# Optimization experiments

Measured on AMD Instinct MI355X. Metric: run time of the kernel, lower is better.

Reference implementation:

```python
import jax, jax.numpy as jnp
import numpy as np

B, N, HID, EPOCH = 16, 512, 32, 201


def setup_inputs() -> dict:
    key = jax.random.key(0)
    k1, k2, k3, k4 = jax.random.split(key, 4)
    f = jax.random.normal(k1, (B, 1, N, N), dtype=jnp.float32)
    # per-sample 3x3 stencil: perturbed 5-point Laplacian, positive center for stable Jacobi
    base = jnp.array([[0., -1., 0.], [-1., 4., -1.], [0., -1., 0.]], dtype=jnp.float32)
    kernelA = base[None, None] + 0.1 * jax.random.normal(k2, (B, 1, 3, 3), dtype=jnp.float32)
    kernelA = kernelA.at[:, :, 1, 1].set(jnp.maximum(kernelA[:, :, 1, 1], 1.0))
    u = jnp.zeros((B, 1, N, N), jnp.float32)
    # stand-in DeepONet H: pointwise 2 -> HID -> 1 MLP on concat(LFA, residual)
    W1 = 0.1 * jax.random.normal(k3, (HID, 2), dtype=jnp.float32)
    b1 = jnp.zeros((HID,), jnp.float32)
    W2 = 0.1 * jax.random.normal(k4, (1, HID), dtype=jnp.float32)
    b2 = jnp.zeros((1,), jnp.float32)
    return {"f": f, "kernelA": kernelA, "u": u, "W1": W1, "b1": b1, "W2": W2, "b2": b2, "epoch": EPOCH}


def _A(x, kernel):
    # per-sample 3x3 stencil: batch dim mapped to channels, grouped conv (groups = B)
    bsz = x.shape[0]
    y = jax.lax.conv_general_dilated(
        jnp.transpose(x, (1, 0, 2, 3)), kernel, (1, 1), ((1, 1), (1, 1)),
        dimension_numbers=("NCHW", "OIHW", "NCHW"), feature_group_count=bsz)
    return jnp.transpose(y, (1, 0, 2, 3))


def _lfa(kernelA, n):
    # ComputeSmootherFactor: Jacobi symbol |prod_j (1 - tau * A_hat(theta))| on the frequency grid
    h = 1.0 / (n + 1)
    p = np.arange(-(n // 2), n // 2)
    P1, P2 = np.meshgrid(p, p)
    t1 = jnp.asarray(2j * np.pi * h * P1, jnp.complex64)
    t2 = jnp.asarray(2j * np.pi * h * P2, jnp.complex64)
    E = jnp.stack([
        jnp.exp(-t1 - t2), jnp.exp(-t2), jnp.exp(t1 - t2),
        jnp.exp(-t1), jnp.ones_like(t1), jnp.exp(t1),
        jnp.exp(-t1 + t2), jnp.exp(t2), jnp.exp(t1 + t2)])  # [9,N,N]
    bsz = kernelA.shape[0]
    S = jnp.einsum("bk,kxy->bxy", kernelA.reshape(bsz, 9).astype(jnp.complex64), E)
    tau = (0.5 / kernelA[:, 0, 1, 1]).astype(jnp.complex64)[:, None, None]
    y = (1.0 - tau * S) ** 5  # 5 identical Jacobi factors
    return jnp.abs(y)[:, None].astype(jnp.float32)  # [B,1,N,N]


def _H(lfa, r, W1, b1, W2, b2):
    # pointwise MLP correction operator (stand-in for DeepONet)
    z = jnp.concatenate([lfa, r], axis=1)  # [B,2,N,N]
    hdn = jax.nn.gelu(jnp.einsum("bcxy,oc->boxy", z, W1) + b1[None, :, None, None])
    return jnp.einsum("bcxy,oc->boxy", hdn, W2) + b2[None, :, None, None]


def reference(f, kernelA, u, W1, b1, W2, b2, epoch):
    K = (epoch - 1) // 100 + 1
    n = f.shape[-1]
    lfa = _lfa(kernelA, n)
    taus = 0.5 / kernelA[:, :, 1:2, 1:2]  # [B,1,1,1], w=0.5
    x = jnp.zeros_like(f)
    for _ in range(K):
        for _ in range(10):  # jacobi, M=10
            x = x + taus * (f - _A(x, kernelA))
        r = f - _A(x, kernelA)
        x = x + _H(lfa, r, W1, b1, W2, b2)
    r = f - _A(x, kernelA)
    return jnp.linalg.norm(r) / jnp.linalg.norm(f)
```

## Files before the change

kernel.cpp:

```cpp
#include <hip/hip_runtime.h>
#include <math.h>

#define BB 16
#define NN 512
#define HID 32

#define HALO 16
#define TW 96
#define TWP 97
#define OT 64

#define GELU_K1 (-2.302208201f)
#define GELU_K2 (-0.102944244f)

#define TPH 0.012247925f
#define CDR 0.99992499f
#define SDR 0.012247618f

template <bool FIRST, bool RES>
__global__ __launch_bounds__(256) void fused_cycle(
        const float* __restrict__ xin, float* __restrict__ xout,
        const float* __restrict__ f, const float* __restrict__ kernelA,
        float* __restrict__ lfa,
        const float* __restrict__ W1, const float* __restrict__ b1,
        const float* __restrict__ W2, const float* __restrict__ b2,
        float* __restrict__ accp) {
    __shared__ float sxraw[98 * TWP + 2];
    float* sx = sxraw + TWP + 1;
    const int tx = threadIdx.x;
    const int ty = threadIdx.y;
    const int t  = ty * 32 + tx;
    const int b  = blockIdx.z;
    const int gy0 = blockIdx.y * OT;
    const int gx0 = blockIdx.x * OT;
    const int goi = gy0 - HALO;
    const int goj = gx0 - HALO;
    const float* fg = f + (size_t)b * NN * NN;
    const float* ag = kernelA + b * 9;
    const float ar0 = ag[0], ar1 = ag[1], ar2 = ag[2], ar3 = ag[3], ar4 = ag[4];
    const float ar5 = ag[5], ar6 = ag[6], ar7 = ag[7], ar8 = ag[8];
    const float tau = 0.5f / ar4;
    const float s0 = tau * ar0, q1 = tau * ar1, q2 = tau * ar2, q3 = tau * ar3;
    const float q4 = tau * ar4, q5 = tau * ar5, q6 = tau * ar6, q7 = tau * ar7;
    const float q8 = tau * ar8;

    if (FIRST) {
        if (t == 0 && (blockIdx.x | blockIdx.y | blockIdx.z) == 0) {
            accp[0] = 0.f;
            accp[1] = 0.f;
        }
        const int orw = t >> 2;
        const int osg = t & 3;
        const int gi_ = gy0 + orw;
        const int gj_ = gx0 + osg * 16;
        const float A35 = ar3 + ar5, A17 = ar1 + ar7, A08 = ar0 + ar8, A26 = ar2 + ar6;
        const float B53 = ar5 - ar3, B71 = ar7 - ar1, B80 = ar8 - ar0, B26 = ar2 - ar6;
        float th2 = TPH * (float)(gi_ - NN / 2);
        float s2v, c2v;
        sincosf(th2, &s2v, &c2v);
        float* lrow = lfa + (size_t)b * NN * NN + (size_t)gi_ * NN + gj_;
        for (int g = 0; g < 4; ++g) {
            float th1 = TPH * (float)(gj_ + g * 4 - NN / 2);
            float s1, c1;
            sincosf(th1, &s1, &c1);
            float out[4];
#pragma unroll
            for (int k = 0; k < 4; ++k) {
                float cc = c1 * c2v, ss = s1 * s2v, sc = s1 * c2v, cs = c1 * s2v;
                float cpp = cc - ss, cpm = cc + ss, spp = sc + cs, spm = sc - cs;
                float re = fmaf(A35, c1, ar4); re = fmaf(A17, c2v, re);
                re = fmaf(A08, cpp, re);       re = fmaf(A26, cpm, re);
                float im = B53 * s1;           im = fmaf(B71, s2v, im);
                im = fmaf(B80, spp, im);       im = fmaf(B26, spm, im);
                float zre = fmaf(-tau, re, 1.0f);
                float zim = tau * im;
                float m2 = fmaf(zre, zre, zim * zim);
                out[k] = m2 * m2 * sqrtf(m2);
                float tt = s1 * SDR;
                float ns = fmaf(s1, CDR, c1 * SDR);
                c1 = fmaf(c1, CDR, -tt);
                s1 = ns;
            }
            float4 ov = {out[0], out[1], out[2], out[3]};
            *(float4*)(lrow + g * 4) = ov;
        }
    }

    if (t < 98) sxraw[t] = 0.f;
    if (t < 96) sxraw[97 + 97 * t] = 0.f;
    if (t < 98) sxraw[9409 + t] = 0.f;

    if (!FIRST) {
        const float* xg = xin + (size_t)b * NN * NN;
#pragma unroll
        for (int k = 0; k < (TW * TW) / 256; ++k) {
            int idx = t + k * 256;
            int row = idx / TW, col = idx - row * TW;
            int gi = goi + row, gj = goj + col;
            float v = 0.f;
            if (gi >= 0 && gi < NN && gj >= 0 && gj < NN) v = xg[gi * NN + gj];
            sx[row * TWP + col] = v;
        }
    }

    const int R0 = ty * 12, C0 = tx * 3;

    const float* pb  = sx + (R0 - 1) * TWP + (C0 - 1);
    float*       pwv = sx + R0 * TWP + C0;

    float vR[12], vC[3];
#pragma unroll
    for (int r = 0; r < 12; ++r) {
        int R = R0 + r, gi = goi + R;
        vR[r] = (R >= 1 && R < TW - 1 && gi >= 0 && gi < NN) ? 1.f : 0.f;
    }
#pragma unroll
    for (int c = 0; c < 3; ++c) {
        int C = C0 + c, gj = goj + C;
        vC[c] = (C >= 1 && C < TW - 1 && gj >= 0 && gj < NN) ? 1.f : 0.f;
    }

    float frt[12][3];
#pragma unroll
    for (int r = 0; r < 12; ++r) {
        int gi = goi + R0 + r;
#pragma unroll
        for (int c = 0; c < 3; ++c) {
            int gj = goj + C0 + c;
            frt[r][c] = (gi >= 0 && gi < NN && gj >= 0 && gj < NN)
                            ? tau * fg[gi * NN + gj] : 0.f;
        }
    }

    __syncthreads();

    float cur[12][3];
    if (FIRST) {
#pragma unroll
        for (int r = 0; r < 12; ++r) {
#pragma unroll
            for (int c = 0; c < 3; ++c)
                cur[r][c] = (vR[r] * vC[c]) * frt[r][c];
        }
        pwv[0] = cur[0][0]; pwv[1] = cur[0][1]; pwv[2] = cur[0][2];
        pwv[11 * TWP] = cur[11][0]; pwv[11 * TWP + 1] = cur[11][1];
        pwv[11 * TWP + 2] = cur[11][2];
#pragma unroll
        for (int r = 1; r < 11; ++r) {
            pwv[r * TWP] = cur[r][0];
            pwv[r * TWP + 2] = cur[r][2];
        }
        __syncthreads();
    } else {
#pragma unroll
        for (int r = 0; r < 12; ++r) {
            cur[r][0] = pwv[r * TWP];
            cur[r][1] = pwv[r * TWP + 1];
            cur[r][2] = pwv[r * TWP + 2];
        }
    }

    for (int s = FIRST ? 1 : 0; s < 10; ++s) {
        float top0 = pb[0], top1 = pb[1], top2 = pb[2], top3 = pb[3], top4 = pb[4];
        float bot0 = pb[13 * TWP],     bot1 = pb[13 * TWP + 1],
              bot2 = pb[13 * TWP + 2], bot3 = pb[13 * TWP + 3],
              bot4 = pb[13 * TWP + 4];
        float pm0 = top1, pm1v = top2, pm2 = top3;
        float Lm1 = top0, Rm1 = top4;
        float Lc = pb[TWP], Rc = pb[TWP + 4];
#pragma unroll
        for (int r = 0; r < 12; ++r) {
            float n0, n1, n2, Lp, Rp;
            if (r < 11) {
                n0 = cur[r + 1][0]; n1 = cur[r + 1][1]; n2 = cur[r + 1][2];
                Lp = pb[(r + 2) * TWP];
                Rp = pb[(r + 2) * TWP + 4];
            } else {
                n0 = bot1; n1 = bot2; n2 = bot3; Lp = bot0; Rp = bot4;
            }
            float o0 = cur[r][0], o1 = cur[r][1], o2 = cur[r][2];
            {
                float ax = s0 * Lm1;
                ax = fmaf(q1, pm0, ax); ax = fmaf(q2, pm1v, ax);
                ax = fmaf(q3, Lc, ax);  ax = fmaf(q4, o0, ax);
                ax = fmaf(q5, o1, ax);  ax = fmaf(q6, Lp, ax);
                ax = fmaf(q7, n0, ax);  ax = fmaf(q8, n1, ax);
                cur[r][0] = fmaf(vR[r] * vC[0], frt[r][0] - ax, o0);
            }
            {
                float ax = s0 * pm0;
                ax = fmaf(q1, pm1v, ax); ax = fmaf(q2, pm2, ax);
                ax = fmaf(q3, o0, ax);   ax = fmaf(q4, o1, ax);
                ax = fmaf(q5, o2, ax);   ax = fmaf(q6, n0, ax);
                ax = fmaf(q7, n1, ax);   ax = fmaf(q8, n2, ax);
                cur[r][1] = fmaf(vR[r] * vC[1], frt[r][1] - ax, o1);
            }
            {
                float ax = s0 * pm1v;
                ax = fmaf(q1, pm2, ax); ax = fmaf(q2, Rm1, ax);
                ax = fmaf(q3, o1, ax);  ax = fmaf(q4, o2, ax);
                ax = fmaf(q5, Rc, ax);  ax = fmaf(q6, n1, ax);
                ax = fmaf(q7, n2, ax);  ax = fmaf(q8, Rp, ax);
                cur[r][2] = fmaf(vR[r] * vC[2], frt[r][2] - ax, o2);
            }
            pm0 = o0; pm1v = o1; pm2 = o2;
            Lm1 = Lc; Rm1 = Rc; Lc = Lp; Rc = Rp;
        }
        __syncthreads();
        if (s < 9) {
            pwv[0] = cur[0][0]; pwv[1] = cur[0][1]; pwv[2] = cur[0][2];
            pwv[11 * TWP] = cur[11][0]; pwv[11 * TWP + 1] = cur[11][1];
            pwv[11 * TWP + 2] = cur[11][2];
#pragma unroll
            for (int r = 1; r < 11; ++r) {
                pwv[r * TWP] = cur[r][0];
                pwv[r * TWP + 2] = cur[r][2];
            }
        } else {
#pragma unroll
            for (int r = 0; r < 12; ++r) {
                pwv[r * TWP] = cur[r][0];
                pwv[r * TWP + 1] = cur[r][1];
                pwv[r * TWP + 2] = cur[r][2];
            }
        }
        __syncthreads();
    }

    const int orow = t >> 2;
    const int oseg = t & 3;
    const int Rl = HALO + orow;
    const int Cl0 = HALO + oseg * 16;
    const float* pw = sx + (Rl - 1) * TWP + (Cl0 - 1);
    const int gi = gy0 + orow;
    const int gjb = gx0 + oseg * 16;
    const float b2v = b2[0];

    if (!RES) {
        float w0[18], w1[18], w2[18];
#pragma unroll
        for (int k = 0; k < 18; ++k) {
            w0[k] = pw[k];
            w1[k] = pw[TWP + k];
            w2[k] = pw[2 * TWP + k];
        }
        const float4* f4 = (const float4*)(fg + (size_t)gi * NN + gjb);
        const float4* l4 = (const float4*)(lfa + (size_t)b * NN * NN + (size_t)gi * NN + gjb);
        float fv[16], lv[16];
#pragma unroll
        for (int q = 0; q < 4; ++q) {
            float4 fq = f4[q], lq = l4[q];
            fv[q * 4] = fq.x; fv[q * 4 + 1] = fq.y; fv[q * 4 + 2] = fq.z; fv[q * 4 + 3] = fq.w;
            lv[q * 4] = lq.x; lv[q * 4 + 1] = lq.y; lv[q * 4 + 2] = lq.z; lv[q * 4 + 3] = lq.w;
        }
        float rv[16];
#pragma unroll
        for (int k = 0; k < 16; ++k) {
            float ax = ar0 * w0[k];
            ax = fmaf(ar1, w0[k + 1], ax); ax = fmaf(ar2, w0[k + 2], ax);
            ax = fmaf(ar3, w1[k], ax);     ax = fmaf(ar4, w1[k + 1], ax);
            ax = fmaf(ar5, w1[k + 2], ax); ax = fmaf(ar6, w2[k], ax);
            ax = fmaf(ar7, w2[k + 1], ax); ax = fmaf(ar8, w2[k + 2], ax);
            rv[k] = fv[k] - ax;
        }
        float acc[16];
#pragma unroll
        for (int k = 0; k < 16; ++k) acc[k] = 0.f;
        for (int hh = 0; hh < HID; ++hh) {
            float w1a = W1[2 * hh], w1b = W1[2 * hh + 1], bb = b1[hh], wo = W2[hh];
#pragma unroll
            for (int k = 0; k < 16; ++k) {
                float v = fmaf(w1a, lv[k], fmaf(w1b, rv[k], bb));
                float m = v * fmaf(GELU_K2, v * v, GELU_K1);
                float e = __builtin_amdgcn_exp2f(m);
                float g = v * __builtin_amdgcn_rcpf(1.0f + e);
                acc[k] = fmaf(wo, g, acc[k]);
            }
        }
        float4* xo4 = (float4*)(xout + (size_t)b * NN * NN + (size_t)gi * NN + gjb);
#pragma unroll
        for (int q = 0; q < 4; ++q) {
            float4 ov;
            ov.x = w1[q * 4 + 1] + acc[q * 4] + b2v;
            ov.y = w1[q * 4 + 2] + acc[q * 4 + 1] + b2v;
            ov.z = w1[q * 4 + 3] + acc[q * 4 + 2] + b2v;
            ov.w = w1[q * 4 + 4] + acc[q * 4 + 3] + b2v;
            xo4[q] = ov;
        }
    } else {
        float rv[16];
        {
            float w[18];
#pragma unroll
            for (int k = 0; k < 18; ++k) w[k] = pw[k];
#pragma unroll
            for (int k = 0; k < 16; ++k) {
                float ax = ar0 * w[k];
                ax = fmaf(ar1, w[k + 1], ax);
                rv[k] = fmaf(ar2, w[k + 2], ax);
            }
#pragma unroll
            for (int k = 0; k < 18; ++k) w[k] = pw[TWP + k];
#pragma unroll
            for (int k = 0; k < 16; ++k) {
                float ax = fmaf(ar3, w[k], rv[k]);
                ax = fmaf(ar4, w[k + 1], ax);
                rv[k] = fmaf(ar5, w[k + 2], ax);
            }
#pragma unroll
            for (int k = 0; k < 18; ++k) w[k] = pw[2 * TWP + k];
#pragma unroll
            for (int k = 0; k < 16; ++k) {
                float ax = fmaf(ar6, w[k], rv[k]);
                ax = fmaf(ar7, w[k + 1], ax);
                rv[k] = fmaf(ar8, w[k + 2], ax);
            }
        }
        float f2 = 0.f;
        {
            const float4* f4 = (const float4*)(fg + (size_t)gi * NN + gjb);
#pragma unroll
            for (int q = 0; q < 4; ++q) {
                float4 fq = f4[q];
                rv[q * 4]     = fq.x - rv[q * 4];
                rv[q * 4 + 1] = fq.y - rv[q * 4 + 1];
                rv[q * 4 + 2] = fq.z - rv[q * 4 + 2];
                rv[q * 4 + 3] = fq.w - rv[q * 4 + 3];
                f2 = fmaf(fq.x, fq.x, f2);
                f2 = fmaf(fq.y, fq.y, f2);
                f2 = fmaf(fq.z, fq.z, f2);
                f2 = fmaf(fq.w, fq.w, f2);
            }
        }

        float Hr0 = 0.f, Hr1 = 0.f;
        int hoff0 = 0, hoff1 = 0;
        auto ringH = [&](int rc, float& Hv, int& hoff) {
            int R, C;
            if (rc < 66)       { R = 15; C = 15 + rc; }
            else if (rc < 132) { R = 80; C = rc - 51; }
            else if (rc < 196) { R = rc - 116; C = 15; }
            else               { R = rc - 180; C = 80; }
            hoff = R * TWP + C;
            int rgi = goi + R, rgj = goj + C;
            Hv = 0.f;
            if (rgi >= 0 && rgi < NN && rgj >= 0 && rgj < NN) {
                const float* pr = sx + (R - 1) * TWP + (C - 1);
                float u0 = pr[0], u1 = pr[1], u2 = pr[2];
                float m0 = pr[TWP], m1 = pr[TWP + 1], m2 = pr[TWP + 2];
                float d0 = pr[2 * TWP], d1 = pr[2 * TWP + 1], d2 = pr[2 * TWP + 2];
                float ax = ar0 * u0;
                ax = fmaf(ar1, u1, ax); ax = fmaf(ar2, u2, ax);
                ax = fmaf(ar3, m0, ax); ax = fmaf(ar4, m1, ax);
                ax = fmaf(ar5, m2, ax); ax = fmaf(ar6, d0, ax);
                ax = fmaf(ar7, d1, ax); ax = fmaf(ar8, d2, ax);
                float rp = fg[(size_t)rgi * NN + rgj] - ax;
                float lf = lfa[(size_t)b * NN * NN + (size_t)rgi * NN + rgj];
                float av = 0.f;
                for (int hh = 0; hh < HID; ++hh) {
                    float w1a = W1[2 * hh], w1b = W1[2 * hh + 1], bbv = b1[hh], wo = W2[hh];
                    float v = fmaf(w1a, lf, fmaf(w1b, rp, bbv));
                    float m = v * fmaf(GELU_K2, v * v, GELU_K1);
                    float e = __builtin_amdgcn_exp2f(m);
                    float gg = v * __builtin_amdgcn_rcpf(1.0f + e);
                    av = fmaf(wo, gg, av);
                }
                Hv = av + b2v;
            }
        };
        ringH(t, Hr0, hoff0);
        if (t < 4) ringH(t + 256, Hr1, hoff1);

        float acc[16];
#pragma unroll
        for (int k = 0; k < 16; ++k) acc[k] = 0.f;
        {
            float lv[16];
            const float4* l4 = (const float4*)(lfa + (size_t)b * NN * NN + (size_t)gi * NN + gjb);
#pragma unroll
            for (int q = 0; q < 4; ++q) {
                float4 lq = l4[q];
                lv[q * 4] = lq.x; lv[q * 4 + 1] = lq.y;
                lv[q * 4 + 2] = lq.z; lv[q * 4 + 3] = lq.w;
            }
            for (int hh = 0; hh < HID; ++hh) {
                float w1a = W1[2 * hh], w1b = W1[2 * hh + 1], bb = b1[hh], wo = W2[hh];
#pragma unroll
                for (int k = 0; k < 16; ++k) {
                    float v = fmaf(w1a, lv[k], fmaf(w1b, rv[k], bb));
                    float m = v * fmaf(GELU_K2, v * v, GELU_K1);
                    float e = __builtin_amdgcn_exp2f(m);
                    float g = v * __builtin_amdgcn_rcpf(1.0f + e);
                    acc[k] = fmaf(wo, g, acc[k]);
                }
            }
        }

        __syncthreads();
        float* ph = sx + Rl * TWP + Cl0;
#pragma unroll
        for (int k = 0; k < 16; ++k) ph[k] = acc[k] + b2v;
        sx[hoff0] = Hr0;
        if (t < 4) sx[hoff1] = Hr1;
        __syncthreads();

        float rr = 0.f;
        {
            float hr[18];
#pragma unroll
            for (int k = 0; k < 18; ++k) hr[k] = pw[k];
#pragma unroll
            for (int k = 0; k < 16; ++k) {
                float ax = ar0 * hr[k];
                ax = fmaf(ar1, hr[k + 1], ax);
                ax = fmaf(ar2, hr[k + 2], ax);
                rv[k] -= ax;
            }
#pragma unroll
            for (int k = 0; k < 18; ++k) hr[k] = pw[TWP + k];
#pragma unroll
            for (int k = 0; k < 16; ++k) {
                float ax = ar3 * hr[k];
                ax = fmaf(ar4, hr[k + 1], ax);
                ax = fmaf(ar5, hr[k + 2], ax);
                rv[k] -= ax;
            }
#pragma unroll
            for (int k = 0; k < 18; ++k) hr[k] = pw[2 * TWP + k];
#pragma unroll
            for (int k = 0; k < 16; ++k) {
                float ax = ar6 * hr[k];
                ax = fmaf(ar7, hr[k + 1], ax);
                ax = fmaf(ar8, hr[k + 2], ax);
                float r = rv[k] - ax;
                rr = fmaf(r, r, rr);
            }
        }
#pragma unroll
        for (int off = 32; off > 0; off >>= 1) {
            rr += __shfl_down(rr, off, 64);
            f2 += __shfl_down(f2, off, 64);
        }
        if ((t & 63) == 0) { sxraw[t >> 6] = rr; sxraw[4 + (t >> 6)] = f2; }
        __syncthreads();
        if (t == 0) {
            atomicAdd(&accp[0], sxraw[0] + sxraw[1] + sxraw[2] + sxraw[3]);
            atomicAdd(&accp[1], sxraw[4] + sxraw[5] + sxraw[6] + sxraw[7]);
        }
    }
}

__global__ void finalize_kernel(const float* __restrict__ acc, float* __restrict__ out) {
    out[0] = sqrtf(acc[0] / acc[1]);
}

extern "C" void kernel_launch(void* const* d_in, const int* in_sizes, int n_in,
                              void* d_out, int out_size, void* d_ws, size_t ws_size,
                              hipStream_t stream) {
    const float* f  = (const float*)d_in[0];
    const float* kA = (const float*)d_in[1];
    float*       u  = (float*)d_in[2];
    const float* W1 = (const float*)d_in[3];
    const float* b1 = (const float*)d_in[4];
    const float* W2 = (const float*)d_in[5];
    const float* b2 = (const float*)d_in[6];
    float* out = (float*)d_out;

    char* ws = (char*)d_ws;
    float* acc = (float*)ws;
    float* xB  = (float*)(ws + 256);
    float* lfa = (float*)(ws + 256 + (size_t)BB * NN * NN * 4);

    dim3 jblk(32, 8);
    dim3 jgrd(NN / OT, NN / OT, BB);

    fused_cycle<true,  false><<<jgrd, jblk, 0, stream>>>(u, xB, f, kA, lfa, W1, b1, W2, b2, acc);
    fused_cycle<false, false><<<jgrd, jblk, 0, stream>>>(xB, u, f, kA, lfa, W1, b1, W2, b2, acc);
    fused_cycle<false, true ><<<jgrd, jblk, 0, stream>>>(u, xB, f, kA, lfa, W1, b1, W2, b2, acc);

    finalize_kernel<<<1, 1, 0, stream>>>(acc, out);
}
```

Measured before the change: 414.3 us.

## Recompute LFA symbol on the fly and fold finalize into last block

Drops the global LFA buffer. The Jacobi smoothing symbol is now recomputed from sincos wherever it is needed: in both H evaluations and in the halo-ring H computations. This removes a 16 MB write and two reads in exchange for extra transcendental and ALU work per cycle. The separate finalize kernel is also removed by having the last block, found through an atomic counter, compute the norm ratio, which saves one launch.

Measured after the change: 511.0 us. 23.3% more time.

```diff
diff --git a/kernel.cpp b/kernel.cpp
--- a/kernel.cpp
+++ b/kernel.cpp
@@ -21,10 +21,9 @@
 __global__ __launch_bounds__(256) void fused_cycle(
         const float* __restrict__ xin, float* __restrict__ xout,
         const float* __restrict__ f, const float* __restrict__ kernelA,
-        float* __restrict__ lfa,
         const float* __restrict__ W1, const float* __restrict__ b1,
         const float* __restrict__ W2, const float* __restrict__ b2,
-        float* __restrict__ accp) {
+        float* __restrict__ accp, float* __restrict__ outp) {
     __shared__ float sxraw[98 * TWP + 2];
     float* sx = sxraw + TWP + 1;
     const int tx = threadIdx.x;
@@ -43,46 +42,14 @@
     const float s0 = tau * ar0, q1 = tau * ar1, q2 = tau * ar2, q3 = tau * ar3;
     const float q4 = tau * ar4, q5 = tau * ar5, q6 = tau * ar6, q7 = tau * ar7;
     const float q8 = tau * ar8;
+    const float A35 = ar3 + ar5, A17 = ar1 + ar7, A08 = ar0 + ar8, A26 = ar2 + ar6;
+    const float B53 = ar5 - ar3, B71 = ar7 - ar1, B80 = ar8 - ar0, B26 = ar2 - ar6;
 
     if (FIRST) {
         if (t == 0 && (blockIdx.x | blockIdx.y | blockIdx.z) == 0) {
             accp[0] = 0.f;
             accp[1] = 0.f;
-        }
-        const int orw = t >> 2;
-        const int osg = t & 3;
-        const int gi_ = gy0 + orw;
-        const int gj_ = gx0 + osg * 16;
-        const float A35 = ar3 + ar5, A17 = ar1 + ar7, A08 = ar0 + ar8, A26 = ar2 + ar6;
-        const float B53 = ar5 - ar3, B71 = ar7 - ar1, B80 = ar8 - ar0, B26 = ar2 - ar6;
-        float th2 = TPH * (float)(gi_ - NN / 2);
-        float s2v, c2v;
-        sincosf(th2, &s2v, &c2v);
-        float* lrow = lfa + (size_t)b * NN * NN + (size_t)gi_ * NN + gj_;
-        for (int g = 0; g < 4; ++g) {
-            float th1 = TPH * (float)(gj_ + g * 4 - NN / 2);
-            float s1, c1;
-            sincosf(th1, &s1, &c1);
-            float out[4];
-#pragma unroll
-            for (int k = 0; k < 4; ++k) {
-                float cc = c1 * c2v, ss = s1 * s2v, sc = s1 * c2v, cs = c1 * s2v;
-                float cpp = cc - ss, cpm = cc + ss, spp = sc + cs, spm = sc - cs;
-                float re = fmaf(A35, c1, ar4); re = fmaf(A17, c2v, re);
-                re = fmaf(A08, cpp, re);       re = fmaf(A26, cpm, re);
-                float im = B53 * s1;           im = fmaf(B71, s2v, im);
-                im = fmaf(B80, spp, im);       im = fmaf(B26, spm, im);
-                float zre = fmaf(-tau, re, 1.0f);
-                float zim = tau * im;
-                float m2 = fmaf(zre, zre, zim * zim);
-                out[k] = m2 * m2 * sqrtf(m2);
-                float tt = s1 * SDR;
-                float ns = fmaf(s1, CDR, c1 * SDR);
-                c1 = fmaf(c1, CDR, -tt);
-                s1 = ns;
-            }
-            float4 ov = {out[0], out[1], out[2], out[3]};
-            *(float4*)(lrow + g * 4) = ov;
+            ((unsigned int*)accp)[2] = 0u;
         }
     }
 
@@ -244,24 +211,53 @@
             w1[k] = pw[TWP + k];
             w2[k] = pw[2 * TWP + k];
         }
-        const float4* f4 = (const float4*)(fg + (size_t)gi * NN + gjb);
-        const float4* l4 = (const float4*)(lfa + (size_t)b * NN * NN + (size_t)gi * NN + gjb);
-        float fv[16], lv[16];
-#pragma unroll
-        for (int q = 0; q < 4; ++q) {
-            float4 fq = f4[q], lq = l4[q];
-            fv[q * 4] = fq.x; fv[q * 4 + 1] = fq.y; fv[q * 4 + 2] = fq.z; fv[q * 4 + 3] = fq.w;
-            lv[q * 4] = lq.x; lv[q * 4 + 1] = lq.y; lv[q * 4 + 2] = lq.z; lv[q * 4 + 3] = lq.w;
-        }
         float rv[16];
-#pragma unroll
-        for (int k = 0; k < 16; ++k) {
-            float ax = ar0 * w0[k];
-            ax = fmaf(ar1, w0[k + 1], ax); ax = fmaf(ar2, w0[k + 2], ax);
-            ax = fmaf(ar3, w1[k], ax);     ax = fmaf(ar4, w1[k + 1], ax);
-            ax = fmaf(ar5, w1[k + 2], ax); ax = fmaf(ar6, w2[k], ax);
-            ax = fmaf(ar7, w2[k + 1], ax); ax = fmaf(ar8, w2[k + 2], ax);
-            rv[k] = fv[k] - ax;
+        {
+            const float4* f4 = (const float4*)(fg + (size_t)gi * NN + gjb);
+            float fv[16];
+#pragma unroll
+            for (int q = 0; q < 4; ++q) {
+                float4 fq = f4[q];
+                fv[q * 4] = fq.x; fv[q * 4 + 1] = fq.y;
+                fv[q * 4 + 2] = fq.z; fv[q * 4 + 3] = fq.w;
+            }
+#pragma unroll
+            for (int k = 0; k < 16; ++k) {
+                float ax = ar0 * w0[k];
+                ax = fmaf(ar1, w0[k + 1], ax); ax = fmaf(ar2, w0[k + 2], ax);
+                ax = fmaf(ar3, w1[k], ax);     ax = fmaf(ar4, w1[k + 1], ax);
+                ax = fmaf(ar5, w1[k + 2], ax); ax = fmaf(ar6, w2[k], ax);
+                ax = fmaf(ar7, w2[k + 1], ax); ax = fmaf(ar8, w2[k + 2], ax);
+                rv[k] = fv[k] - ax;
+            }
+        }
+        float lv[16];
+        {
+            float th2 = TPH * (float)(gi - NN / 2);
+            float s2v, c2v;
+            sincosf(th2, &s2v, &c2v);
+            for (int g = 0; g < 4; ++g) {
+                float th1 = TPH * (float)(gjb + g * 4 - NN / 2);
+                float s1, c1;
+                sincosf(th1, &s1, &c1);
+#pragma unroll
+                for (int k = 0; k < 4; ++k) {
+                    float cc = c1 * c2v, ss = s1 * s2v, sc = s1 * c2v, cs = c1 * s2v;
+                    float cpp = cc - ss, cpm = cc + ss, spp = sc + cs, spm = sc - cs;
+                    float re = fmaf(A35, c1, ar4); re = fmaf(A17, c2v, re);
+                    re = fmaf(A08, cpp, re);       re = fmaf(A26, cpm, re);
+                    float im = B53 * s1;           im = fmaf(B71, s2v, im);
+                    im = fmaf(B80, spp, im);       im = fmaf(B26, spm, im);
+                    float zre = fmaf(-tau, re, 1.0f);
+                    float zim = tau * im;
+                    float m2 = fmaf(zre, zre, zim * zim);
+                    lv[g * 4 + k] = m2 * m2 * sqrtf(m2);
+                    float tt = s1 * SDR;
+                    float ns = fmaf(s1, CDR, c1 * SDR);
+                    c1 = fmaf(c1, CDR, -tt);
+                    s1 = ns;
+                }
+            }
         }
         float acc[16];
 #pragma unroll
@@ -355,7 +351,32 @@
                 ax = fmaf(ar5, m2, ax); ax = fmaf(ar6, d0, ax);
                 ax = fmaf(ar7, d1, ax); ax = fmaf(ar8, d2, ax);
                 float rp = fg[(size_t)rgi * NN + rgj] - ax;
-                float lf = lfa[(size_t)b * NN * NN + (size_t)rgi * NN + rgj];
+                float lf;
+                {
+                    float th2 = TPH * (float)(rgi - NN / 2);
+                    float s2v, c2v;
+                    sincosf(th2, &s2v, &c2v);
+                    float th1 = TPH * (float)((rgj & ~3) - NN / 2);
+                    float s1, c1;
+                    sincosf(th1, &s1, &c1);
+                    int rmd = rgj & 3;
+                    for (int k = 0; k < rmd; ++k) {
+                        float tt = s1 * SDR;
+                        float ns = fmaf(s1, CDR, c1 * SDR);
+                        c1 = fmaf(c1, CDR, -tt);
+                        s1 = ns;
+                    }
+                    float cc = c1 * c2v, ss = s1 * s2v, sc = s1 * c2v, cs = c1 * s2v;
+                    float cpp = cc - ss, cpm = cc + ss, spp = sc + cs, spm = sc - cs;
+                    float re = fmaf(A35, c1, ar4); re = fmaf(A17, c2v, re);
+                    re = fmaf(A08, cpp, re);       re = fmaf(A26, cpm, re);
+                    float im = B53 * s1;           im = fmaf(B71, s2v, im);
+                    im = fmaf(B80, spp, im);       im = fmaf(B26, spm, im);
+                    float zre = fmaf(-tau, re, 1.0f);
+                    float zim = tau * im;
+                    float m2 = fmaf(zre, zre, zim * zim);
+                    lf = m2 * m2 * sqrtf(m2);
+                }
                 float av = 0.f;
                 for (int hh = 0; hh < HID; ++hh) {
                     float w1a = W1[2 * hh], w1b = W1[2 * hh + 1], bbv = b1[hh], wo = W2[hh];
@@ -376,12 +397,32 @@
         for (int k = 0; k < 16; ++k) acc[k] = 0.f;
         {
             float lv[16];
-            const float4* l4 = (const float4*)(lfa + (size_t)b * NN * NN + (size_t)gi * NN + gjb);
-#pragma unroll
-            for (int q = 0; q < 4; ++q) {
-                float4 lq = l4[q];
-                lv[q * 4] = lq.x; lv[q * 4 + 1] = lq.y;
-                lv[q * 4 + 2] = lq.z; lv[q * 4 + 3] = lq.w;
+            {
+                float th2 = TPH * (float)(gi - NN / 2);
+                float s2v, c2v;
+                sincosf(th2, &s2v, &c2v);
+                for (int g = 0; g < 4; ++g) {
+                    float th1 = TPH * (float)(gjb + g * 4 - NN / 2);
+                    float s1, c1;
+                    sincosf(th1, &s1, &c1);
+#pragma unroll
+                    for (int k = 0; k < 4; ++k) {
+                        float cc = c1 * c2v, ss = s1 * s2v, sc = s1 * c2v, cs = c1 * s2v;
+                        float cpp = cc - ss, cpm = cc + ss, spp = sc + cs, spm = sc - cs;
+                        float re = fmaf(A35, c1, ar4); re = fmaf(A17, c2v, re);
+                        re = fmaf(A08, cpp, re);       re = fmaf(A26, cpm, re);
+                        float im = B53 * s1;           im = fmaf(B71, s2v, im);
+                        im = fmaf(B80, spp, im);       im = fmaf(B26, spm, im);
+                        float zre = fmaf(-tau, re, 1.0f);
+                        float zim = tau * im;
+                        float m2 = fmaf(zre, zre, zim * zim);
+                        lv[g * 4 + k] = m2 * m2 * sqrtf(m2);
+                        float tt = s1 * SDR;
+                        float ns = fmaf(s1, CDR, c1 * SDR);
+                        c1 = fmaf(c1, CDR, -tt);
+                        s1 = ns;
+                    }
+                }
             }
             for (int hh = 0; hh < HID; ++hh) {
                 float w1a = W1[2 * hh], w1b = W1[2 * hh + 1], bb = b1[hh], wo = W2[hh];
@@ -446,12 +487,16 @@
         if (t == 0) {
             atomicAdd(&accp[0], sxraw[0] + sxraw[1] + sxraw[2] + sxraw[3]);
             atomicAdd(&accp[1], sxraw[4] + sxraw[5] + sxraw[6] + sxraw[7]);
-        }
-    }
-}
-
-__global__ void finalize_kernel(const float* __restrict__ acc, float* __restrict__ out) {
-    out[0] = sqrtf(acc[0] / acc[1]);
+            __threadfence();
+            unsigned int done = atomicAdd((unsigned int*)accp + 2, 1u);
+            if (done == (NN / OT) * (NN / OT) * BB - 1) {
+                __threadfence();
+                float rrt = atomicAdd(&accp[0], 0.f);
+                float fft = atomicAdd(&accp[1], 0.f);
+                outp[0] = sqrtf(rrt / fft);
+            }
+        }
+    }
 }
 
 extern "C" void kernel_launch(void* const* d_in, const int* in_sizes, int n_in,
@@ -469,14 +514,11 @@
     char* ws = (char*)d_ws;
     float* acc = (float*)ws;
     float* xB  = (float*)(ws + 256);
-    float* lfa = (float*)(ws + 256 + (size_t)BB * NN * NN * 4);
 
     dim3 jblk(32, 8);
     dim3 jgrd(NN / OT, NN / OT, BB);
 
-    fused_cycle<true,  false><<<jgrd, jblk, 0, stream>>>(u, xB, f, kA, lfa, W1, b1, W2, b2, acc);
-    fused_cycle<false, false><<<jgrd, jblk, 0, stream>>>(xB, u, f, kA, lfa, W1, b1, W2, b2, acc);
-    fused_cycle<false, true ><<<jgrd, jblk, 0, stream>>>(u, xB, f, kA, lfa, W1, b1, W2, b2, acc);
-
-    finalize_kernel<<<1, 1, 0, stream>>>(acc, out);
+    fused_cycle<true,  false><<<jgrd, jblk, 0, stream>>>(u, xB, f, kA, W1, b1, W2, b2, acc, out);
+    fused_cycle<false, false><<<jgrd, jblk, 0, stream>>>(xB, u, f, kA, W1, b1, W2, b2, acc, out);
+    fused_cycle<false, true ><<<jgrd, jblk, 0, stream>>>(u, xB, f, kA, W1, b1, W2, b2, acc, out);
 }
```
